# Kernel tuning notes

Hardware: AMD Instinct MI355X
Metric: run time of the kernel (lower is better)

The kernel has to match this reference:

```python
import jax, jax.numpy as jnp
import numpy as np

TEMPERATURE = 0.5


def setup_inputs() -> dict:
    key = jax.random.key(0)
    k1, k2 = jax.random.split(key)
    N, D = 4096, 512
    emb_i = jax.random.normal(k1, (N, D), dtype=jnp.float32)
    emb_j = jax.random.normal(k2, (N, D), dtype=jnp.float32)
    return {"emb_i": emb_i, "emb_j": emb_j}


def reference(emb_i, emb_j):
    # L2-normalize each embedding row (F.normalize, dim=1)
    z_i = emb_i / jnp.linalg.norm(emb_i, axis=1, keepdims=True)
    z_j = emb_j / jnp.linalg.norm(emb_j, axis=1, keepdims=True)
    reps = jnp.concatenate([z_i, z_j], axis=0)  # [2N, D]
    N = emb_i.shape[0]
    M = 2 * N
    # cosine similarity of normalized vectors == dot product -> [2N, 2N]
    sim = jnp.einsum('id,jd->ij', reps, reps) / TEMPERATURE
    # denominator: sum_k!=i exp(sim[i,k]); original multiplies by one-hot complement
    exp_sim = jnp.exp(sim)
    denom = jnp.sum(exp_sim, axis=1) - jnp.diagonal(exp_sim)  # [2N]
    log_denom = jnp.log(denom)
    # positive pairs: (k, k+N) and (k+N, k)
    idx = jnp.arange(N)
    pos_ij = sim[idx, idx + N]          # sim(k, k+N)/T
    pos_ji = sim[idx + N, idx]          # sim(k+N, k)/T
    loss = jnp.sum(-(pos_ij - log_denom[:N]) - (pos_ji - log_denom[N:]))
    return loss / (2.0 * N)
```

## Files before the change

kernel.cpp:

```cpp
#include <hip/hip_runtime.h>
#include <cstdint>
#include <cstddef>

constexpr int N_ROWS = 4096;
constexpr int D      = 512;
constexpr int M      = 8192;
constexpr int NTILE  = 64;
constexpr int NBLK   = NTILE * (NTILE + 1) / 2;
constexpr int BKB    = 64;
constexpr int LDSB   = 128 * BKB;

using f32x4 = __attribute__((ext_vector_type(4))) float;
using ul2   = __attribute__((ext_vector_type(2))) unsigned long;

#define ASYNC_CP16(gsrc, ldst)                                                      \
    __builtin_amdgcn_global_load_lds(                                               \
        (const __attribute__((address_space(1))) unsigned int*)(gsrc),              \
        (__attribute__((address_space(3))) unsigned int*)(ldst), 16, 0, 0)

#define SS_FP8(pk, accum)                                                           \
    do {                                                                            \
        float f0 = __builtin_amdgcn_cvt_f32_fp8((pk), 0);                           \
        float f1 = __builtin_amdgcn_cvt_f32_fp8((pk), 1);                           \
        float f2 = __builtin_amdgcn_cvt_f32_fp8((pk), 2);                           \
        float f3 = __builtin_amdgcn_cvt_f32_fp8((pk), 3);                           \
        (accum) += f0 * f0 + f1 * f1 + f2 * f2 + f3 * f3;                           \
    } while (0)

__global__ __launch_bounds__(256) void normpos_kernel(
    const float* __restrict__ emb_i, const float* __restrict__ emb_j,
    uint8_t* __restrict__ zb, float* __restrict__ diagss,
    float* __restrict__ pos)
{
    const int wave = threadIdx.x >> 6, lane = threadIdx.x & 63;
    const int k = blockIdx.x * 4 + wave;

    const float4* a = (const float4*)(emb_i + (size_t)k * D);
    const float4* b = (const float4*)(emb_j + (size_t)k * D);
    float4 a0 = a[lane * 2], a1 = a[lane * 2 + 1];
    float4 b0 = b[lane * 2], b1 = b[lane * 2 + 1];

    float ssi = a0.x*a0.x + a0.y*a0.y + a0.z*a0.z + a0.w*a0.w
              + a1.x*a1.x + a1.y*a1.y + a1.z*a1.z + a1.w*a1.w;
    float ssj = b0.x*b0.x + b0.y*b0.y + b0.z*b0.z + b0.w*b0.w
              + b1.x*b1.x + b1.y*b1.y + b1.z*b1.z + b1.w*b1.w;
    float dp  = a0.x*b0.x + a0.y*b0.y + a0.z*b0.z + a0.w*b0.w
              + a1.x*b1.x + a1.y*b1.y + a1.z*b1.z + a1.w*b1.w;
    #pragma unroll
    for (int off = 32; off; off >>= 1) {
        ssi += __shfl_xor(ssi, off, 64);
        ssj += __shfl_xor(ssj, off, 64);
        dp  += __shfl_xor(dp,  off, 64);
    }
    const float invi = rsqrtf(ssi), invj = rsqrtf(ssj);

    const float zi[8] = {a0.x*invi, a0.y*invi, a0.z*invi, a0.w*invi,
                         a1.x*invi, a1.y*invi, a1.z*invi, a1.w*invi};
    const float zj[8] = {b0.x*invj, b0.y*invj, b0.z*invj, b0.w*invj,
                         b1.x*invj, b1.y*invj, b1.z*invj, b1.w*invj};

    int pi0 = __builtin_amdgcn_cvt_pk_fp8_f32(zi[0], zi[1], 0, false);
    pi0     = __builtin_amdgcn_cvt_pk_fp8_f32(zi[2], zi[3], pi0, true);
    int pi1 = __builtin_amdgcn_cvt_pk_fp8_f32(zi[4], zi[5], 0, false);
    pi1     = __builtin_amdgcn_cvt_pk_fp8_f32(zi[6], zi[7], pi1, true);
    int pj0 = __builtin_amdgcn_cvt_pk_fp8_f32(zj[0], zj[1], 0, false);
    pj0     = __builtin_amdgcn_cvt_pk_fp8_f32(zj[2], zj[3], pj0, true);
    int pj1 = __builtin_amdgcn_cvt_pk_fp8_f32(zj[4], zj[5], 0, false);
    pj1     = __builtin_amdgcn_cvt_pk_fp8_f32(zj[6], zj[7], pj1, true);

    float dssi = 0.f, dssj = 0.f;
    SS_FP8(pi0, dssi);
    SS_FP8(pi1, dssi);
    SS_FP8(pj0, dssj);
    SS_FP8(pj1, dssj);

    const int g = lane, bb = g >> 3, w = g & 7;
    const int sl = bb * 8 + ((w < 4) ? (w * 2) : ((w - 4) * 2 + 1));
    const unsigned long long vi =
        ((unsigned long long)(unsigned)pi1 << 32) | (unsigned)pi0;
    const unsigned long long vj =
        ((unsigned long long)(unsigned)pj1 << 32) | (unsigned)pj0;
    *(unsigned long long*)(zb + (size_t)k * D + sl * 8)            = vi;
    *(unsigned long long*)(zb + (size_t)(k + N_ROWS) * D + sl * 8) = vj;

    #pragma unroll
    for (int off = 32; off; off >>= 1) {
        dssi += __shfl_xor(dssi, off, 64);
        dssj += __shfl_xor(dssj, off, 64);
    }
    if (lane == 0) {
        diagss[k]          = dssi;
        diagss[k + N_ROWS] = dssj;
        pos[k]             = 2.0f * dp * invi * invj;
    }
}

__global__ __launch_bounds__(256, 4) void simgemm_kernel(
    const uint8_t* __restrict__ zb, float* __restrict__ partials)
{
    __shared__ ul2 AsV[2 * LDSB / 16];
    __shared__ ul2 BsV[2 * LDSB / 16];
    __shared__ float rp[4][64];
    __shared__ float cp4[4][64];
    uint8_t* As = (uint8_t*)AsV;
    uint8_t* Bs = (uint8_t*)BsV;

    const int tid  = threadIdx.x;
    const int wave = tid >> 6, lane = tid & 63;
    const int l15  = lane & 15, ks = lane >> 4;

    const int t = blockIdx.x;
    int bi = (int)((129.0f - sqrtf(129.0f * 129.0f - 8.0f * (float)t)) * 0.5f);
    while (bi > 0 && bi * (129 - bi) / 2 > t) --bi;
    while ((bi + 1) * (129 - (bi + 1)) / 2 <= t) ++bi;
    const int bj = bi + (t - bi * (129 - bi) / 2);
    const bool diag = (bi == bj);

    const int wrow = (wave >> 1) * 64, wcol = (wave & 1) * 64;

    const int srow = wave * 32 + (lane >> 2);
    const int scol = ((lane & 3) ^ ((lane >> 3) & 3)) * 16;
    const uint8_t* gA = zb + (size_t)(bi * 128 + srow) * D + scol;
    const uint8_t* gB = zb + (size_t)(bj * 128 + srow) * D + scol;
    uint8_t* lA = As + wave * 32 * BKB;
    uint8_t* lB = Bs + wave * 32 * BKB;

    ASYNC_CP16(gA,            lA);
    ASYNC_CP16(gA + 16 * D,   lA + 16 * BKB);
    ASYNC_CP16(gB,            lB);
    ASYNC_CP16(gB + 16 * D,   lB + 16 * BKB);

    f32x4 acc[4][4] = {};
    const int swb = (ks ^ ((l15 >> 1) & 3)) * 16;

    for (int it = 0; it < D / BKB; ++it) {
        __syncthreads();

        if (it + 1 < D / BKB) {
            const int kc  = (it + 1) * BKB;
            const int off = ((it + 1) & 1) * LDSB;
            ASYNC_CP16(gA + kc,          lA + off);
            ASYNC_CP16(gA + kc + 16 * D, lA + off + 16 * BKB);
            ASYNC_CP16(gB + kc,          lB + off);
            ASYNC_CP16(gB + kc + 16 * D, lB + off + 16 * BKB);
        }

        const int cb = (it & 1) * LDSB;
        ul2 af[4], bg[4];
        #pragma unroll
        for (int f = 0; f < 4; ++f) {
            af[f] = *(const ul2*)(As + cb + (wrow + f * 16 + l15) * BKB + swb);
            bg[f] = *(const ul2*)(Bs + cb + (wcol + f * 16 + l15) * BKB + swb);
        }
        #pragma unroll
        for (int i = 0; i < 4; ++i)
            #pragma unroll
            for (int j = 0; j < 4; ++j) {
                acc[i][j] = __builtin_amdgcn_mfma_f32_16x16x32_fp8_fp8(
                    (long)af[i][0], (long)bg[j][0], acc[i][j], 0, 0, 0);
                acc[i][j] = __builtin_amdgcn_mfma_f32_16x16x32_fp8_fp8(
                    (long)af[i][1], (long)bg[j][1], acc[i][j], 0, 0, 0);
            }
    }

    float rowp[4][4] = {};
    #pragma unroll
    for (int j = 0; j < 4; ++j) {
        float cpj = 0.f;
        #pragma unroll
        for (int i = 0; i < 4; ++i)
            #pragma unroll
            for (int r = 0; r < 4; ++r) {
                float e = __expf(2.0f * acc[i][j][r]);
                rowp[i][r] += e;
                cpj += e;
            }
        if (!diag) {
            cpj += __shfl_xor(cpj, 16, 64);
            cpj += __shfl_xor(cpj, 32, 64);
            if (ks == 0) cp4[wave][j * 16 + l15] = cpj;
        }
    }
    #pragma unroll
    for (int i = 0; i < 4; ++i)
        #pragma unroll
        for (int r = 0; r < 4; ++r) {
            float e = rowp[i][r];
            e += __shfl_xor(e, 1, 64);
            e += __shfl_xor(e, 2, 64);
            e += __shfl_xor(e, 4, 64);
            e += __shfl_xor(e, 8, 64);
            if (l15 == 0) rp[wave][i * 16 + ks * 4 + r] = e;
        }
    __syncthreads();

    float* pA = partials + (size_t)(bi * NTILE + bj) * 128;
    float* pB = partials + (size_t)(bj * NTILE + bi) * 128;
    if (tid < 128) {
        const int h = tid >> 6, rr = tid & 63;
        pA[tid] = rp[h * 2][rr] + rp[h * 2 + 1][rr];
    } else if (!diag) {
        const int c = tid - 128, h = c >> 6, cc = c & 63;
        pB[c] = cp4[h][cc] + cp4[h + 2][cc];
    }
}

__global__ __launch_bounds__(256) void rowfin_kernel(
    const float* __restrict__ partials, const float* __restrict__ diagss,
    const float* __restrict__ pos, float* __restrict__ lgpart)
{
    const int r  = blockIdx.x;
    const int ri = threadIdx.x & 127;
    const int ch = threadIdx.x >> 7;
    const float* base = partials + (size_t)r * NTILE * 128 + ri;
    float s = 0.f;
    #pragma unroll
    for (int c = 0; c < 32; ++c)
        s += base[(size_t)(ch * 32 + c) * 128];
    __shared__ float half1[128];
    __shared__ float red[4];
    if (ch == 1) half1[ri] = s;
    __syncthreads();
    float lg = 0.f;
    if (ch == 0) {
        float rs = s + half1[ri];
        int row = r * 128 + ri;
        lg = __logf(rs - __expf(2.0f * diagss[row]));
    }
    if (threadIdx.x < 64)
        lg -= 2.0f * pos[r * 64 + threadIdx.x];
    #pragma unroll
    for (int off = 32; off; off >>= 1) lg += __shfl_xor(lg, off, 64);
    const int wave = threadIdx.x >> 6, lane = threadIdx.x & 63;
    if (lane == 0) red[wave] = lg;
    __syncthreads();
    if (threadIdx.x == 0) lgpart[r] = red[0] + red[1] + red[2] + red[3];
}

__global__ __launch_bounds__(64) void loss_kernel(
    const float* __restrict__ lgpart, float* __restrict__ out)
{
    float local = lgpart[threadIdx.x];
    #pragma unroll
    for (int off = 32; off; off >>= 1) local += __shfl_xor(local, off, 64);
    if (threadIdx.x == 0) out[0] = local * (1.0f / 8192.0f);
}

extern "C" void kernel_launch(void* const* d_in, const int* in_sizes, int n_in,
                              void* d_out, int out_size, void* d_ws, size_t ws_size,
                              hipStream_t stream)
{
    const float* emb_i = (const float*)d_in[0];
    const float* emb_j = (const float*)d_in[1];

    uint8_t* zb = (uint8_t*)d_ws;
    float* partials = (float*)((char*)d_ws + (size_t)M * D);
    float* diagss   = partials + (size_t)NTILE * NTILE * 128;
    float* pos      = diagss + M;
    float* lgpart   = pos + N_ROWS;
    float* out      = (float*)d_out;

    normpos_kernel<<<N_ROWS / 4, 256, 0, stream>>>(emb_i, emb_j, zb, diagss, pos);
    simgemm_kernel<<<NBLK, 256, 0, stream>>>(zb, partials);
    rowfin_kernel<<<NTILE, 256, 0, stream>>>(partials, diagss, pos, lgpart);
    loss_kernel<<<1, 64, 0, stream>>>(lgpart, out);
}
```

Before: 103.6 us.

## Switch FP8 sim-GEMM to scaled 16x16x128 MFMA with 128-byte K tiles

Replaces pairs of 16x16x32 FP8 MFMAs with the MI355 block-scaled 16x16x128 f8f6f4 MFMA, using unit scales (0x7F). The K tile doubles to 128 bytes, which halves the main-loop iterations and barriers. The LDS layout moves to an 8-way XOR swizzle, and the prior permuted store order in the normalization kernel is dropped. LDS use doubles, so launch bounds drop to 2 blocks per CU, which reduces occupancy.

```diff
diff --git a/kernel.cpp b/kernel.cpp
--- a/kernel.cpp
+++ b/kernel.cpp
@@ -7,11 +7,12 @@
 constexpr int M      = 8192;
 constexpr int NTILE  = 64;
 constexpr int NBLK   = NTILE * (NTILE + 1) / 2;
-constexpr int BKB    = 64;
+constexpr int BKB    = 128;
 constexpr int LDSB   = 128 * BKB;
 
 using f32x4 = __attribute__((ext_vector_type(4))) float;
-using ul2   = __attribute__((ext_vector_type(2))) unsigned long;
+using i32x4 = __attribute__((ext_vector_type(4))) int;
+using i32x8 = __attribute__((ext_vector_type(8))) int;
 
 #define ASYNC_CP16(gsrc, ldst)                                                      \
     __builtin_amdgcn_global_load_lds(                                               \
@@ -74,14 +75,12 @@
     SS_FP8(pj0, dssj);
     SS_FP8(pj1, dssj);
 
-    const int g = lane, bb = g >> 3, w = g & 7;
-    const int sl = bb * 8 + ((w < 4) ? (w * 2) : ((w - 4) * 2 + 1));
     const unsigned long long vi =
         ((unsigned long long)(unsigned)pi1 << 32) | (unsigned)pi0;
     const unsigned long long vj =
         ((unsigned long long)(unsigned)pj1 << 32) | (unsigned)pj0;
-    *(unsigned long long*)(zb + (size_t)k * D + sl * 8)            = vi;
-    *(unsigned long long*)(zb + (size_t)(k + N_ROWS) * D + sl * 8) = vj;
+    *(unsigned long long*)(zb + (size_t)k * D + lane * 8)            = vi;
+    *(unsigned long long*)(zb + (size_t)(k + N_ROWS) * D + lane * 8) = vj;
 
     #pragma unroll
     for (int off = 32; off; off >>= 1) {
@@ -95,11 +94,11 @@
     }
 }
 
-__global__ __launch_bounds__(256, 4) void simgemm_kernel(
+__global__ __launch_bounds__(256, 2) void simgemm_kernel(
     const uint8_t* __restrict__ zb, float* __restrict__ partials)
 {
-    __shared__ ul2 AsV[2 * LDSB / 16];
-    __shared__ ul2 BsV[2 * LDSB / 16];
+    __shared__ i32x4 AsV[2 * LDSB / 16];
+    __shared__ i32x4 BsV[2 * LDSB / 16];
     __shared__ float rp[4][64];
     __shared__ float cp4[4][64];
     uint8_t* As = (uint8_t*)AsV;
@@ -118,20 +117,20 @@
 
     const int wrow = (wave >> 1) * 64, wcol = (wave & 1) * 64;
 
-    const int srow = wave * 32 + (lane >> 2);
-    const int scol = ((lane & 3) ^ ((lane >> 3) & 3)) * 16;
-    const uint8_t* gA = zb + (size_t)(bi * 128 + srow) * D + scol;
-    const uint8_t* gB = zb + (size_t)(bj * 128 + srow) * D + scol;
+    const int srow = (lane >> 3);
+    const int scol = ((lane & 7) ^ ((lane >> 3) & 7)) * 16;
+    const uint8_t* gA = zb + (size_t)(bi * 128 + wave * 32 + srow) * D + scol;
+    const uint8_t* gB = zb + (size_t)(bj * 128 + wave * 32 + srow) * D + scol;
     uint8_t* lA = As + wave * 32 * BKB;
     uint8_t* lB = Bs + wave * 32 * BKB;
 
-    ASYNC_CP16(gA,            lA);
-    ASYNC_CP16(gA + 16 * D,   lA + 16 * BKB);
-    ASYNC_CP16(gB,            lB);
-    ASYNC_CP16(gB + 16 * D,   lB + 16 * BKB);
+    #pragma unroll
+    for (int c = 0; c < 4; ++c) {
+        ASYNC_CP16(gA + (size_t)c * 8 * D, lA + c * 8 * BKB);
+        ASYNC_CP16(gB + (size_t)c * 8 * D, lB + c * 8 * BKB);
+    }
 
     f32x4 acc[4][4] = {};
-    const int swb = (ks ^ ((l15 >> 1) & 3)) * 16;
 
     for (int it = 0; it < D / BKB; ++it) {
         __syncthreads();
@@ -139,28 +138,42 @@
         if (it + 1 < D / BKB) {
             const int kc  = (it + 1) * BKB;
             const int off = ((it + 1) & 1) * LDSB;
-            ASYNC_CP16(gA + kc,          lA + off);
-            ASYNC_CP16(gA + kc + 16 * D, lA + off + 16 * BKB);
-            ASYNC_CP16(gB + kc,          lB + off);
-            ASYNC_CP16(gB + kc + 16 * D, lB + off + 16 * BKB);
+            #pragma unroll
+            for (int c = 0; c < 4; ++c) {
+                ASYNC_CP16(gA + kc + (size_t)c * 8 * D, lA + off + c * 8 * BKB);
+                ASYNC_CP16(gB + kc + (size_t)c * 8 * D, lB + off + c * 8 * BKB);
+            }
         }
 
         const int cb = (it & 1) * LDSB;
-        ul2 af[4], bg[4];
+        i32x8 af[4], bg[4];
         #pragma unroll
         for (int f = 0; f < 4; ++f) {
-            af[f] = *(const ul2*)(As + cb + (wrow + f * 16 + l15) * BKB + swb);
-            bg[f] = *(const ul2*)(Bs + cb + (wcol + f * 16 + l15) * BKB + swb);
+            {
+                const int R = wrow + f * 16 + l15;
+                const uint8_t* base = As + cb + R * BKB;
+                const int sw = (R & 7);
+                i32x4 lo = *(const i32x4*)(base + ((ks * 2)     ^ sw) * 16);
+                i32x4 hi = *(const i32x4*)(base + ((ks * 2 + 1) ^ sw) * 16);
+                af[f][0] = lo[0]; af[f][1] = lo[1]; af[f][2] = lo[2]; af[f][3] = lo[3];
+                af[f][4] = hi[0]; af[f][5] = hi[1]; af[f][6] = hi[2]; af[f][7] = hi[3];
+            }
+            {
+                const int R = wcol + f * 16 + l15;
+                const uint8_t* base = Bs + cb + R * BKB;
+                const int sw = (R & 7);
+                i32x4 lo = *(const i32x4*)(base + ((ks * 2)     ^ sw) * 16);
+                i32x4 hi = *(const i32x4*)(base + ((ks * 2 + 1) ^ sw) * 16);
+                bg[f][0] = lo[0]; bg[f][1] = lo[1]; bg[f][2] = lo[2]; bg[f][3] = lo[3];
+                bg[f][4] = hi[0]; bg[f][5] = hi[1]; bg[f][6] = hi[2]; bg[f][7] = hi[3];
+            }
         }
         #pragma unroll
         for (int i = 0; i < 4; ++i)
             #pragma unroll
-            for (int j = 0; j < 4; ++j) {
-                acc[i][j] = __builtin_amdgcn_mfma_f32_16x16x32_fp8_fp8(
-                    (long)af[i][0], (long)bg[j][0], acc[i][j], 0, 0, 0);
-                acc[i][j] = __builtin_amdgcn_mfma_f32_16x16x32_fp8_fp8(
-                    (long)af[i][1], (long)bg[j][1], acc[i][j], 0, 0, 0);
-            }
+            for (int j = 0; j < 4; ++j)
+                acc[i][j] = __builtin_amdgcn_mfma_scale_f32_16x16x128_f8f6f4(
+                    af[i], bg[j], acc[i][j], 0, 0, 0, 0x7F, 0, 0x7F);
     }
 
     float rowp[4][4] = {};
```

Result: slower. 111.5 us (+7.6%).
